# Performance work log

Measured on AMD Instinct MI355X. Metric: run time of the kernel, lower is better.

## Reference

```python
import jax, jax.numpy as jnp
import numpy as np

N, B, H, C, NF = 200000, 100, 128, 3, 128


def setup_inputs() -> dict:
    key = jax.random.key(0)
    ks = jax.random.split(key, 12)
    def w(k, shape, s=0.05):
        return jax.random.normal(k, shape, jnp.float32) * s
    return dict(
        node_feat=w(ks[0], (N, NF), 1.0),
        coord=w(ks[1], (N, 3), 1.0),
        virtual_node_feat=w(ks[2], (B, NF, C), 1.0),
        virtual_coord=w(ks[3], (B, 3, C), 1.0),
        data_batch=jnp.sort(jax.random.randint(ks[4], (N,), 0, B)),
        We1=w(ks[5], (2 * NF + 1, H)), be1=jnp.zeros((H,), jnp.float32),
        We2=w(ks[6], (H, H)), be2=jnp.zeros((H,), jnp.float32),
        Wc1=w(ks[7], (H, H)), bc1=jnp.zeros((H,), jnp.float32),
        Wc2=w(ks[8], (H, 1), 0.001),  # xavier gain=0.001 layer, no bias
        Wn1=w(ks[9], (2 * H, H)), bn1=jnp.zeros((H,), jnp.float32),
        Wn2=w(ks[10], (H, H)), bn2=jnp.zeros((H,), jnp.float32),
    )


def _segment_mean(x, idx, num_segments):
    # x: [N, d1, d2] -> [num_segments, d1, d2]; mean over nodes of each graph
    sums = jax.ops.segment_sum(x, idx, num_segments=num_segments)
    counts = jax.ops.segment_sum(jnp.ones((x.shape[0],), x.dtype), idx,
                                 num_segments=num_segments)
    return sums / jnp.maximum(counts, 1.0)[:, None, None]


def reference(node_feat, coord, virtual_node_feat, virtual_coord, data_batch,
              We1, be1, We2, be2, Wc1, bc1, Wc2, Wn1, bn1, Wn2, bn2):
    silu = jax.nn.silu
    n, nf = node_feat.shape
    nb, _, c = virtual_coord.shape

    # gather: real node -> its graph's virtual nodes
    diff = virtual_coord[data_batch] - coord[:, :, None]            # [N,3,C]
    radial = jnp.linalg.norm(diff, axis=1)                          # [N,C]

    # edge model (work in [N,C,feat] layout to avoid permutes)
    feat_R = jnp.broadcast_to(node_feat[:, None, :], (n, c, nf))    # [N,C,NF]
    feat_V = virtual_node_feat[data_batch].transpose(0, 2, 1)       # [N,C,NF]
    e_in = jnp.concatenate([feat_R, feat_V, radial[:, :, None]], axis=-1)
    m = silu(e_in @ We1 + be1)
    m = silu(m @ We2 + be2)                                         # [N,C,H]

    # coord model: per (node, virtual-channel) scalar weight
    s = silu(m @ Wc1 + bc1) @ Wc2                                   # [N,C,1]
    trans = diff * s[:, :, 0][:, None, :]                           # [N,3,C]
    virtual_coord = virtual_coord + _segment_mean(trans, data_batch, nb)

    # node model on virtual nodes
    agg = _segment_mean(m, data_batch, nb)                          # [B,C,H]
    n_in = jnp.concatenate([virtual_node_feat.transpose(0, 2, 1), agg], axis=-1)
    h = silu(n_in @ Wn1 + bn1) @ Wn2 + bn2                          # [B,C,H]
    virtual_node_feat = virtual_node_feat + h.transpose(0, 2, 1)    # residual

    return virtual_node_feat, virtual_coord
```

## Files before the change

kernel.cpp:

```cpp
#include <hip/hip_runtime.h>
#include <hip/hip_bf16.h>
#include <math.h>

#define NNODES 200000
#define NGRAPH 100
#define HD     128
#define NCH    3
#define BN     64
#define EROWS  (BN*NCH)
#define ESTR   136

typedef short short8 __attribute__((ext_vector_type(8)));
typedef float f32x4  __attribute__((ext_vector_type(4)));
typedef unsigned int u32x2 __attribute__((ext_vector_type(2)));
typedef unsigned int u32x4 __attribute__((ext_vector_type(4)));

#define MFMA_16x16x32(a,b,c) __builtin_amdgcn_mfma_f32_16x16x32_bf16((a),(b),(c),0,0,0)

__device__ __forceinline__ float bf2f(unsigned short u) {
    return __uint_as_float(((unsigned int)u) << 16);
}
__device__ __forceinline__ unsigned short f2bf(float f) {
    return (unsigned short)((__float_as_uint(f) + 0x8000u) >> 16);
}
__device__ __forceinline__ unsigned int pack2bf(float lo, float hi) {
    unsigned int a = __float_as_uint(lo) + 0x8000u;
    unsigned int b = __float_as_uint(hi) + 0x8000u;
    return __builtin_amdgcn_perm(b, a, 0x07060302u);
}
__device__ __forceinline__ short8 as_short8(u32x4 v) {
    union { u32x4 u; short8 s; } x; x.u = v; return x.s;
}
__device__ __forceinline__ float silu_f(float x) {
    return x * __builtin_amdgcn_rcpf(1.0f + __expf(-x));
}

__global__ void prep_kernel(const float* __restrict__ We1,
                            const float* __restrict__ We2,
                            const float* __restrict__ Wc1,
                            const float* __restrict__ be1,
                            const float* __restrict__ be2,
                            const float* __restrict__ bc1,
                            const float* __restrict__ Wc2,
                            const float* __restrict__ vnf,
                            unsigned short* __restrict__ w1r,
                            unsigned short* __restrict__ w2r,
                            unsigned short* __restrict__ wc1r,
                            float* __restrict__ Q,
                            float* __restrict__ wlast,
                            float* __restrict__ be1f,
                            float* __restrict__ be2f,
                            float* __restrict__ bc1f,
                            float* __restrict__ wc2f,
                            float* __restrict__ zacc) {
    int bid = blockIdx.x;
    if (bid < 192) {
        int t = bid * 256 + threadIdx.x;
        int m  = t / 16384;
        int e  = t % 16384;
        int j  = e & 7;
        int l  = (e >> 3) & 63;
        int ks = (e >> 9) & 3;
        int ct = e >> 11;
        int kf  = ks * 32 + (l >> 4) * 8 + j;
        int col = ct * 16 + (l & 15);
        int srck = (m == 0) ? kf : (((kf & 7) << 4) | (kf >> 3));
        const float*    src = (m == 0) ? We1 : ((m == 1) ? We2 : Wc1);
        unsigned short* dst = (m == 0) ? w1r : ((m == 1) ? w2r : wc1r);
        dst[e] = f2bf(src[srck * 128 + col]);
        if (t < 128) {
            wlast[t] = We1[256 * 128 + t];
            be1f[t]  = be1[t];
            be2f[t]  = be2[t];
            bc1f[t]  = bc1[t];
            wc2f[t]  = Wc2[t];
        }
    } else if (bid < 492) {
        int bc = bid - 192;
        int b = bc / NCH, c = bc % NCH;
        int t = threadIdx.x;
        __shared__ float v[128];
        if (t < 128) v[t] = vnf[(b * 128 + t) * 3 + c];
        __syncthreads();
        if (t < 128) {
            float s0 = 0.f, s1 = 0.f, s2 = 0.f, s3 = 0.f;
            for (int k = 0; k < 128; k += 4) {
                s0 += v[k + 0] * We1[(128 + k + 0) * 128 + t];
                s1 += v[k + 1] * We1[(128 + k + 1) * 128 + t];
                s2 += v[k + 2] * We1[(128 + k + 2) * 128 + t];
                s3 += v[k + 3] * We1[(128 + k + 3) * 128 + t];
            }
            Q[(b * 3 + c) * 128 + t] = (s0 + s1) + (s2 + s3);
        }
    } else {
        int idx = (bid - 492) * 256 + threadIdx.x;
        if (idx < 39400) zacc[idx] = 0.0f;
    }
}

__global__ __launch_bounds__(256, 2) void egcl_main(
    const float* __restrict__ node_feat,
    const float* __restrict__ coord,
    const float* __restrict__ vcoord,
    const int*   __restrict__ batch,
    const unsigned short* __restrict__ w1r,
    const unsigned short* __restrict__ w2r,
    const unsigned short* __restrict__ wc1r,
    const float* __restrict__ Q,
    const float* __restrict__ wlast,
    const float* __restrict__ be1f,
    const float* __restrict__ be2f,
    const float* __restrict__ bc1f,
    const float* __restrict__ wc2f,
    float* __restrict__ aggsum,
    float* __restrict__ transsum,
    float* __restrict__ cnt)
{
    __shared__ __align__(16) unsigned short e_buf[EROWS * ESTR];
    __shared__ unsigned short sbatch[BN];
    __shared__ unsigned short sseg_start[BN + 1];
    __shared__ unsigned short sseg_b[BN];
    __shared__ int snseg;

    const int tid   = threadIdx.x;
    const int wave  = tid >> 6;
    const int lane  = tid & 63;
    const int lrow  = lane & 15;
    const int lkb   = (lane >> 4) * 8;
    const int rq    = (lane >> 4) * 4;
    const int node0 = blockIdx.x * BN;

    if (tid < BN) {
        int n = node0 + tid;
        int b = batch[n];
        sbatch[tid] = (unsigned short)b;
        int prev = (tid > 0) ? batch[n - 1] : -1;
        unsigned long long mask = __ballot(b != prev);
        int ns = __popcll(mask);
        if (b != prev) {
            int idx = __popcll(mask & ((1ull << tid) - 1ull));
            sseg_start[idx] = (unsigned short)tid;
            sseg_b[idx]     = (unsigned short)b;
        }
        if (tid == 0) { sseg_start[ns] = BN; snseg = ns; }
        float cx = coord[n * 3 + 0];
        float cy = coord[n * 3 + 1];
        float cz = coord[n * 3 + 2];
        for (int c = 0; c < 3; ++c) {
            float dx = vcoord[b * 9 + 0 * 3 + c] - cx;
            float dy = vcoord[b * 9 + 1 * 3 + c] - cy;
            float dz = vcoord[b * 9 + 2 * 3 + c] - cz;
            f32x4 pad;
            pad[0] = dx; pad[1] = dy; pad[2] = dz;
            pad[3] = sqrtf(dx * dx + dy * dy + dz * dz);
            *(f32x4*)&e_buf[(c * 64 + tid) * ESTR + 128] = pad;
        }
    }
    __syncthreads();
    const int nseg = snseg;

    f32x4 acc1[8] = {};
    {
        const float* arow = node_feat + (size_t)(node0 + wave * 16 + lrow) * 128;
        for (int ks = 0; ks < 4; ++ks) {
            f32x4 x0 = *(const f32x4*)(arow + ks * 32 + lkb);
            f32x4 x1 = *(const f32x4*)(arow + ks * 32 + lkb + 4);
            u32x4 av;
            av[0] = pack2bf(x0[0], x0[1]);
            av[1] = pack2bf(x0[2], x0[3]);
            av[2] = pack2bf(x1[0], x1[1]);
            av[3] = pack2bf(x1[2], x1[3]);
            short8 af = as_short8(av);
            for (int ct = 0; ct < 8; ++ct) {
                short8 bfg = *(const short8*)(w1r + ((ct * 4 + ks) * 64 + lane) * 8);
                acc1[ct] = MFMA_16x16x32(af, bfg, acc1[ct]);
            }
        }
    }
    {
        float wl[8];
        #pragma unroll
        for (int ct = 0; ct < 8; ++ct)
            wl[ct] = wlast[ct * 16 + lrow];
        if (nseg == 1) {
            const float* qb = Q + (int)sseg_b[0] * (NCH * HD);
            float qv[3][8];
            #pragma unroll
            for (int c = 0; c < 3; ++c)
                #pragma unroll
                for (int ct = 0; ct < 8; ++ct)
                    qv[c][ct] = qb[c * 128 + ct * 16 + lrow] + be1f[ct * 16 + lrow];
            #pragma unroll
            for (int r = 0; r < 4; ++r) {
                int nl = wave * 16 + rq + r;
                #pragma unroll
                for (int c = 0; c < 3; ++c) {
                    int row = c * 64 + nl;
                    float rad = *(const float*)&e_buf[row * ESTR + 134];
                    float v[8];
                    #pragma unroll
                    for (int ct = 0; ct < 8; ++ct)
                        v[ct] = silu_f(acc1[ct][r] + qv[c][ct] + rad * wl[ct]);
                    u32x4 av;
                    av[0] = pack2bf(v[0], v[1]);
                    av[1] = pack2bf(v[2], v[3]);
                    av[2] = pack2bf(v[4], v[5]);
                    av[3] = pack2bf(v[6], v[7]);
                    *(u32x4*)&e_buf[row * ESTR + lrow * 8] = av;
                }
            }
        } else {
            float bb[8];
            #pragma unroll
            for (int ct = 0; ct < 8; ++ct)
                bb[ct] = be1f[ct * 16 + lrow];
            #pragma unroll
            for (int r = 0; r < 4; ++r) {
                int nl = wave * 16 + rq + r;
                int b  = sbatch[nl];
                #pragma unroll
                for (int c = 0; c < 3; ++c) {
                    int row = c * 64 + nl;
                    float rad = *(const float*)&e_buf[row * ESTR + 134];
                    const float* qb = Q + (b * 3 + c) * 128;
                    float v[8];
                    #pragma unroll
                    for (int ct = 0; ct < 8; ++ct)
                        v[ct] = silu_f(acc1[ct][r] + bb[ct] + qb[ct * 16 + lrow]
                                       + rad * wl[ct]);
                    u32x4 av;
                    av[0] = pack2bf(v[0], v[1]);
                    av[1] = pack2bf(v[2], v[3]);
                    av[2] = pack2bf(v[4], v[5]);
                    av[3] = pack2bf(v[6], v[7]);
                    *(u32x4*)&e_buf[row * ESTR + lrow * 8] = av;
                }
            }
        }
    }

    const int bagg = (nseg == 1) ? (int)sseg_b[0] * (NCH * HD) : 0;

    for (int half = 0; half < 2; ++half) {
        f32x4 acc[3][4] = {};
        for (int ks = 0; ks < 4; ++ks) {
            short8 af[3];
            #pragma unroll
            for (int j = 0; j < 3; ++j)
                af[j] = *(const short8*)(&e_buf[(j * 64 + wave * 16 + lrow) * ESTR +
                                                ks * 32 + lkb]);
            #pragma unroll
            for (int c4 = 0; c4 < 4; ++c4) {
                int ct = half * 4 + c4;
                short8 bfg = *(const short8*)(w2r + ((ct * 4 + ks) * 64 + lane) * 8);
                #pragma unroll
                for (int j = 0; j < 3; ++j)
                    acc[j][c4] = MFMA_16x16x32(af[j], bfg, acc[j][c4]);
            }
        }
        float b0 = be2f[(half * 4 + 0) * 16 + lrow];
        float b1 = be2f[(half * 4 + 1) * 16 + lrow];
        float b2 = be2f[(half * 4 + 2) * 16 + lrow];
        float b3 = be2f[(half * 4 + 3) * 16 + lrow];
        #pragma unroll
        for (int j = 0; j < 3; ++j) {
            float ps0 = 0.f, ps1 = 0.f, ps2 = 0.f, ps3 = 0.f;
            #pragma unroll
            for (int r = 0; r < 4; ++r) {
                int row = j * 64 + wave * 16 + rq + r;
                float v0 = silu_f(acc[j][0][r] + b0);
                float v1 = silu_f(acc[j][1][r] + b1);
                float v2 = silu_f(acc[j][2][r] + b2);
                float v3 = silu_f(acc[j][3][r] + b3);
                ps0 += v0; ps1 += v1; ps2 += v2; ps3 += v3;
                u32x2 dv;
                dv[0] = pack2bf(v0, v1);
                dv[1] = pack2bf(v2, v3);
                *(u32x2*)&e_buf[row * ESTR + lrow * 8 + half * 4] = dv;
            }
            if (nseg == 1) {
                ps0 += __shfl_xor(ps0, 16, 64); ps0 += __shfl_xor(ps0, 32, 64);
                ps1 += __shfl_xor(ps1, 16, 64); ps1 += __shfl_xor(ps1, 32, 64);
                ps2 += __shfl_xor(ps2, 16, 64); ps2 += __shfl_xor(ps2, 32, 64);
                ps3 += __shfl_xor(ps3, 16, 64); ps3 += __shfl_xor(ps3, 32, 64);
                if (lane < 16) {
                    atomicAdd(&aggsum[bagg + j * 128 + (half * 4 + 0) * 16 + lane], ps0);
                    atomicAdd(&aggsum[bagg + j * 128 + (half * 4 + 1) * 16 + lane], ps1);
                    atomicAdd(&aggsum[bagg + j * 128 + (half * 4 + 2) * 16 + lane], ps2);
                    atomicAdd(&aggsum[bagg + j * 128 + (half * 4 + 3) * 16 + lane], ps3);
                }
            }
        }
    }

    float p[3][4] = {};
    for (int half = 0; half < 2; ++half) {
        f32x4 acc[3][4] = {};
        for (int ks = 0; ks < 4; ++ks) {
            short8 af[3];
            #pragma unroll
            for (int j = 0; j < 3; ++j)
                af[j] = *(const short8*)(&e_buf[(j * 64 + wave * 16 + lrow) * ESTR +
                                                ks * 32 + lkb]);
            #pragma unroll
            for (int c4 = 0; c4 < 4; ++c4) {
                int ct = half * 4 + c4;
                short8 bfg = *(const short8*)(wc1r + ((ct * 4 + ks) * 64 + lane) * 8);
                #pragma unroll
                for (int j = 0; j < 3; ++j)
                    acc[j][c4] = MFMA_16x16x32(af[j], bfg, acc[j][c4]);
            }
        }
        float b0 = bc1f[(half * 4 + 0) * 16 + lrow];
        float b1 = bc1f[(half * 4 + 1) * 16 + lrow];
        float b2 = bc1f[(half * 4 + 2) * 16 + lrow];
        float b3 = bc1f[(half * 4 + 3) * 16 + lrow];
        float w0 = wc2f[(half * 4 + 0) * 16 + lrow];
        float w1 = wc2f[(half * 4 + 1) * 16 + lrow];
        float w2 = wc2f[(half * 4 + 2) * 16 + lrow];
        float w3 = wc2f[(half * 4 + 3) * 16 + lrow];
        #pragma unroll
        for (int j = 0; j < 3; ++j) {
            #pragma unroll
            for (int r = 0; r < 4; ++r) {
                float s = p[j][r];
                s += silu_f(acc[j][0][r] + b0) * w0;
                s += silu_f(acc[j][1][r] + b1) * w1;
                s += silu_f(acc[j][2][r] + b2) * w2;
                s += silu_f(acc[j][3][r] + b3) * w3;
                p[j][r] = s;
            }
        }
    }
    for (int j = 0; j < 3; ++j) {
        float p0 = p[j][0], p1 = p[j][1], p2 = p[j][2], p3 = p[j][3];
        #pragma unroll
        for (int off = 1; off < 16; off <<= 1) {
            p0 += __shfl_xor(p0, off, 64);
            p1 += __shfl_xor(p1, off, 64);
            p2 += __shfl_xor(p2, off, 64);
            p3 += __shfl_xor(p3, off, 64);
        }
        if (lrow == 0) {
            int rbase = j * 64 + wave * 16 + rq;
            *(float*)&e_buf[(rbase + 0) * ESTR + 134] = p0;
            *(float*)&e_buf[(rbase + 1) * ESTR + 134] = p1;
            *(float*)&e_buf[(rbase + 2) * ESTR + 134] = p2;
            *(float*)&e_buf[(rbase + 3) * ESTR + 134] = p3;
        }
    }
    __syncthreads();

    if (nseg == 1) {
        int b = sseg_b[0];
        if (wave == 0) {
            float t[9];
            #pragma unroll
            for (int c = 0; c < 3; ++c) {
                int row = c * 64 + lane;
                float sv = *(const float*)&e_buf[row * ESTR + 134];
                float dx = *(const float*)&e_buf[row * ESTR + 128];
                float dy = *(const float*)&e_buf[row * ESTR + 130];
                float dz = *(const float*)&e_buf[row * ESTR + 132];
                t[0 * 3 + c] = dx * sv;
                t[1 * 3 + c] = dy * sv;
                t[2 * 3 + c] = dz * sv;
            }
            #pragma unroll
            for (int off = 1; off < 64; off <<= 1)
                #pragma unroll
                for (int k = 0; k < 9; ++k)
                    t[k] += __shfl_xor(t[k], off, 64);
            if (lane < 9)
                atomicAdd(&transsum[b * 9 + lane],
                          __shfl(t[lane], 0, 64));
            if (lane == 0) atomicAdd(&cnt[b], 64.0f);
        }
    } else {
        for (int sg = 0; sg < nseg; ++sg) {
            int s0 = sseg_start[sg], s1 = sseg_start[sg + 1], b = sseg_b[sg];
            for (int idx = tid; idx < NCH * HD; idx += 256) {
                int c = idx >> 7, pcol = idx & 127;
                float sum = 0.f;
                for (int ii = s0; ii < s1; ++ii)
                    sum += bf2f(e_buf[(c * 64 + ii) * ESTR + pcol]);
                int h = ((pcol & 7) << 4) | (pcol >> 3);
                atomicAdd(&aggsum[(b * 3 + c) * 128 + h], sum);
            }
            if (tid < 9) {
                int d = tid / 3, c = tid % 3;
                float sum = 0.f;
                for (int ii = s0; ii < s1; ++ii)
                    sum += (*(const float*)&e_buf[(c * 64 + ii) * ESTR + 128 + 2 * d])
                           * (*(const float*)&e_buf[(c * 64 + ii) * ESTR + 134]);
                atomicAdd(&transsum[b * 9 + d * 3 + c], sum);
            }
            if (tid == 0) atomicAdd(&cnt[b], (float)(s1 - s0));
        }
    }
}

__global__ void finalize_kernel(const float* __restrict__ vnf,
                                const float* __restrict__ vcoord,
                                const float* __restrict__ Wn1,
                                const float* __restrict__ bn1,
                                const float* __restrict__ Wn2,
                                const float* __restrict__ bn2,
                                const float* __restrict__ aggsum,
                                const float* __restrict__ transsum,
                                const float* __restrict__ cnt,
                                float* __restrict__ out) {
    int b = blockIdx.x / NCH;
    int c = blockIdx.x % NCH;
    int j = threadIdx.x;
    __shared__ float nin[256];
    __shared__ float h1[128];
    float count = fmaxf(cnt[b], 1.0f);
    nin[j]       = vnf[(b * 128 + j) * 3 + c];
    nin[128 + j] = aggsum[(b * 3 + c) * 128 + j] / count;
    __syncthreads();
    float x0 = bn1[j], x1 = 0.f, x2 = 0.f, x3 = 0.f;
    for (int k = 0; k < 256; k += 4) {
        x0 += nin[k + 0] * Wn1[(k + 0) * 128 + j];
        x1 += nin[k + 1] * Wn1[(k + 1) * 128 + j];
        x2 += nin[k + 2] * Wn1[(k + 2) * 128 + j];
        x3 += nin[k + 3] * Wn1[(k + 3) * 128 + j];
    }
    h1[j] = silu_f((x0 + x1) + (x2 + x3));
    __syncthreads();
    float y0 = bn2[j], y1 = 0.f, y2 = 0.f, y3 = 0.f;
    for (int k = 0; k < 128; k += 4) {
        y0 += h1[k + 0] * Wn2[(k + 0) * 128 + j];
        y1 += h1[k + 1] * Wn2[(k + 1) * 128 + j];
        y2 += h1[k + 2] * Wn2[(k + 2) * 128 + j];
        y3 += h1[k + 3] * Wn2[(k + 3) * 128 + j];
    }
    float y = (y0 + y1) + (y2 + y3);
    out[(b * 128 + j) * 3 + c] = vnf[(b * 128 + j) * 3 + c] + y;
    if (c == 0 && j < 9) {
        out[NGRAPH * 128 * 3 + b * 9 + j] =
            vcoord[b * 9 + j] + transsum[b * 9 + j] / count;
    }
}

extern "C" void kernel_launch(void* const* d_in, const int* in_sizes, int n_in,
                              void* d_out, int out_size, void* d_ws, size_t ws_size,
                              hipStream_t stream) {
    const float* node_feat = (const float*)d_in[0];
    const float* coord     = (const float*)d_in[1];
    const float* vnf       = (const float*)d_in[2];
    const float* vcoord    = (const float*)d_in[3];
    const int*   batch     = (const int*)d_in[4];
    const float* We1 = (const float*)d_in[5];
    const float* be1 = (const float*)d_in[6];
    const float* We2 = (const float*)d_in[7];
    const float* be2 = (const float*)d_in[8];
    const float* Wc1 = (const float*)d_in[9];
    const float* bc1 = (const float*)d_in[10];
    const float* Wc2 = (const float*)d_in[11];
    const float* Wn1 = (const float*)d_in[12];
    const float* bn1 = (const float*)d_in[13];
    const float* Wn2 = (const float*)d_in[14];
    const float* bn2 = (const float*)d_in[15];

    char* ws = (char*)d_ws;
    float*          aggsum   = (float*)(ws + 0);
    float*          transsum = (float*)(ws + 153600);
    float*          cntp     = (float*)(ws + 157200);
    float*          Q        = (float*)(ws + 157600);
    unsigned short* w1r      = (unsigned short*)(ws + 311200);
    unsigned short* w2r      = (unsigned short*)(ws + 343968);
    unsigned short* wc1r     = (unsigned short*)(ws + 376736);
    float*          wlast    = (float*)(ws + 409504);
    float*          be1f     = (float*)(ws + 410016);
    float*          be2f     = (float*)(ws + 410528);
    float*          bc1f     = (float*)(ws + 411040);
    float*          wc2f     = (float*)(ws + 411552);

    prep_kernel<<<192 + NGRAPH * NCH + 154, 256, 0, stream>>>(
        We1, We2, Wc1, be1, be2, bc1, Wc2, vnf,
        w1r, w2r, wc1r, Q, wlast, be1f, be2f, bc1f, wc2f,
        (float*)ws);

    egcl_main<<<NNODES / BN, 256, 0, stream>>>(
        node_feat, coord, vcoord, batch, w1r, w2r, wc1r, Q,
        wlast, be1f, be2f, bc1f, wc2f, aggsum, transsum, cntp);

    finalize_kernel<<<NGRAPH * NCH, 128, 0, stream>>>(
        vnf, vcoord, Wn1, bn1, Wn2, bn2, aggsum, transsum, cntp,
        (float*)d_out);
}
```

Before: 299.4 us.

## Shrink LDS footprint by processing channel 2 in a second pass

The edge staging buffer drops from three channel planes to two. The third channel's layer-1 output is held in registers and processed after channels 0 and 1 finish layer 2 and the coord MLP. Radial and diff values and the per-row scalars move into small separate float buffers. The aim is to cut shared memory per block so more blocks fit per CU and register pressure in the MFMA loops falls, at the cost of redoing the weight loads for a third pass and adding extra barriers when a tile holds several segments.

```diff
diff --git a/kernel.cpp b/kernel.cpp
--- a/kernel.cpp
+++ b/kernel.cpp
@@ -9,6 +9,7 @@
 #define BN     64
 #define EROWS  (BN*NCH)
 #define ESTR   136
+#define PL     (BN*ESTR)
 
 typedef short short8 __attribute__((ext_vector_type(8)));
 typedef float f32x4  __attribute__((ext_vector_type(4)));
@@ -116,7 +117,9 @@
     float* __restrict__ transsum,
     float* __restrict__ cnt)
 {
-    __shared__ __align__(16) unsigned short e_buf[EROWS * ESTR];
+    __shared__ __align__(16) unsigned short planes[2][PL];
+    __shared__ __align__(16) float pad_buf[EROWS * 4];
+    __shared__ float s_vals[EROWS];
     __shared__ unsigned short sbatch[BN];
     __shared__ unsigned short sseg_start[BN + 1];
     __shared__ unsigned short sseg_b[BN];
@@ -129,6 +132,7 @@
     const int lkb   = (lane >> 4) * 8;
     const int rq    = (lane >> 4) * 4;
     const int node0 = blockIdx.x * BN;
+    const int myrow = wave * 16 + lrow;
 
     if (tid < BN) {
         int n = node0 + tid;
@@ -153,7 +157,7 @@
             f32x4 pad;
             pad[0] = dx; pad[1] = dy; pad[2] = dz;
             pad[3] = sqrtf(dx * dx + dy * dy + dz * dz);
-            *(f32x4*)&e_buf[(c * 64 + tid) * ESTR + 128] = pad;
+            *(f32x4*)&pad_buf[(c * 64 + tid) * 4] = pad;
         }
     }
     __syncthreads();
@@ -161,7 +165,7 @@
 
     f32x4 acc1[8] = {};
     {
-        const float* arow = node_feat + (size_t)(node0 + wave * 16 + lrow) * 128;
+        const float* arow = node_feat + (size_t)(node0 + myrow) * 128;
         for (int ks = 0; ks < 4; ++ks) {
             f32x4 x0 = *(const f32x4*)(arow + ks * 32 + lkb);
             f32x4 x1 = *(const f32x4*)(arow + ks * 32 + lkb + 4);
@@ -177,13 +181,17 @@
             }
         }
     }
+
+    const int bagg = (nseg == 1) ? (int)sseg_b[0] * (NCH * HD) : 0;
+
+    u32x4 e2r[4];
     {
         float wl[8];
         #pragma unroll
         for (int ct = 0; ct < 8; ++ct)
             wl[ct] = wlast[ct * 16 + lrow];
         if (nseg == 1) {
-            const float* qb = Q + (int)sseg_b[0] * (NCH * HD);
+            const float* qb = Q + bagg;
             float qv[3][8];
             #pragma unroll
             for (int c = 0; c < 3; ++c)
@@ -195,8 +203,7 @@
                 int nl = wave * 16 + rq + r;
                 #pragma unroll
                 for (int c = 0; c < 3; ++c) {
-                    int row = c * 64 + nl;
-                    float rad = *(const float*)&e_buf[row * ESTR + 134];
+                    float rad = pad_buf[(c * 64 + nl) * 4 + 3];
                     float v[8];
                     #pragma unroll
                     for (int ct = 0; ct < 8; ++ct)
@@ -206,7 +213,8 @@
                     av[1] = pack2bf(v[2], v[3]);
                     av[2] = pack2bf(v[4], v[5]);
                     av[3] = pack2bf(v[6], v[7]);
-                    *(u32x4*)&e_buf[row * ESTR + lrow * 8] = av;
+                    if (c < 2) *(u32x4*)&planes[c][nl * ESTR + lrow * 8] = av;
+                    else       e2r[r] = av;
                 }
             }
         } else {
@@ -220,8 +228,7 @@
                 int b  = sbatch[nl];
                 #pragma unroll
                 for (int c = 0; c < 3; ++c) {
-                    int row = c * 64 + nl;
-                    float rad = *(const float*)&e_buf[row * ESTR + 134];
+                    float rad = pad_buf[(c * 64 + nl) * 4 + 3];
                     const float* qb = Q + (b * 3 + c) * 128;
                     float v[8];
                     #pragma unroll
@@ -233,29 +240,25 @@
                     av[1] = pack2bf(v[2], v[3]);
                     av[2] = pack2bf(v[4], v[5]);
                     av[3] = pack2bf(v[6], v[7]);
-                    *(u32x4*)&e_buf[row * ESTR + lrow * 8] = av;
+                    if (c < 2) *(u32x4*)&planes[c][nl * ESTR + lrow * 8] = av;
+                    else       e2r[r] = av;
                 }
             }
         }
     }
-
-    const int bagg = (nseg == 1) ? (int)sseg_b[0] * (NCH * HD) : 0;
+    asm volatile("" ::: "memory");
 
     for (int half = 0; half < 2; ++half) {
-        f32x4 acc[3][4] = {};
+        f32x4 acc[2][4] = {};
         for (int ks = 0; ks < 4; ++ks) {
-            short8 af[3];
-            #pragma unroll
-            for (int j = 0; j < 3; ++j)
-                af[j] = *(const short8*)(&e_buf[(j * 64 + wave * 16 + lrow) * ESTR +
-                                                ks * 32 + lkb]);
+            short8 af0 = *(const short8*)&planes[0][myrow * ESTR + ks * 32 + lkb];
+            short8 af1 = *(const short8*)&planes[1][myrow * ESTR + ks * 32 + lkb];
             #pragma unroll
             for (int c4 = 0; c4 < 4; ++c4) {
                 int ct = half * 4 + c4;
                 short8 bfg = *(const short8*)(w2r + ((ct * 4 + ks) * 64 + lane) * 8);
-                #pragma unroll
-                for (int j = 0; j < 3; ++j)
-                    acc[j][c4] = MFMA_16x16x32(af[j], bfg, acc[j][c4]);
+                acc[0][c4] = MFMA_16x16x32(af0, bfg, acc[0][c4]);
+                acc[1][c4] = MFMA_16x16x32(af1, bfg, acc[1][c4]);
             }
         }
         float b0 = be2f[(half * 4 + 0) * 16 + lrow];
@@ -263,11 +266,11 @@
         float b2 = be2f[(half * 4 + 2) * 16 + lrow];
         float b3 = be2f[(half * 4 + 3) * 16 + lrow];
         #pragma unroll
-        for (int j = 0; j < 3; ++j) {
+        for (int j = 0; j < 2; ++j) {
             float ps0 = 0.f, ps1 = 0.f, ps2 = 0.f, ps3 = 0.f;
             #pragma unroll
             for (int r = 0; r < 4; ++r) {
-                int row = j * 64 + wave * 16 + rq + r;
+                int nl = wave * 16 + rq + r;
                 float v0 = silu_f(acc[j][0][r] + b0);
                 float v1 = silu_f(acc[j][1][r] + b1);
                 float v2 = silu_f(acc[j][2][r] + b2);
@@ -276,7 +279,7 @@
                 u32x2 dv;
                 dv[0] = pack2bf(v0, v1);
                 dv[1] = pack2bf(v2, v3);
-                *(u32x2*)&e_buf[row * ESTR + lrow * 8 + half * 4] = dv;
+                *(u32x2*)&planes[j][nl * ESTR + lrow * 8 + half * 4] = dv;
             }
             if (nseg == 1) {
                 ps0 += __shfl_xor(ps0, 16, 64); ps0 += __shfl_xor(ps0, 32, 64);
@@ -292,48 +295,148 @@
             }
         }
     }
-
-    float p[3][4] = {};
-    for (int half = 0; half < 2; ++half) {
-        f32x4 acc[3][4] = {};
+    asm volatile("" ::: "memory");
+
+    {
+        float p[2][4] = {};
+        for (int half = 0; half < 2; ++half) {
+            f32x4 acc[2][4] = {};
+            for (int ks = 0; ks < 4; ++ks) {
+                short8 af0 = *(const short8*)&planes[0][myrow * ESTR + ks * 32 + lkb];
+                short8 af1 = *(const short8*)&planes[1][myrow * ESTR + ks * 32 + lkb];
+                #pragma unroll
+                for (int c4 = 0; c4 < 4; ++c4) {
+                    int ct = half * 4 + c4;
+                    short8 bfg = *(const short8*)(wc1r + ((ct * 4 + ks) * 64 + lane) * 8);
+                    acc[0][c4] = MFMA_16x16x32(af0, bfg, acc[0][c4]);
+                    acc[1][c4] = MFMA_16x16x32(af1, bfg, acc[1][c4]);
+                }
+            }
+            float b0 = bc1f[(half * 4 + 0) * 16 + lrow];
+            float b1 = bc1f[(half * 4 + 1) * 16 + lrow];
+            float b2 = bc1f[(half * 4 + 2) * 16 + lrow];
+            float b3 = bc1f[(half * 4 + 3) * 16 + lrow];
+            float w0 = wc2f[(half * 4 + 0) * 16 + lrow];
+            float w1 = wc2f[(half * 4 + 1) * 16 + lrow];
+            float w2 = wc2f[(half * 4 + 2) * 16 + lrow];
+            float w3 = wc2f[(half * 4 + 3) * 16 + lrow];
+            #pragma unroll
+            for (int j = 0; j < 2; ++j) {
+                #pragma unroll
+                for (int r = 0; r < 4; ++r) {
+                    float s = p[j][r];
+                    s += silu_f(acc[j][0][r] + b0) * w0;
+                    s += silu_f(acc[j][1][r] + b1) * w1;
+                    s += silu_f(acc[j][2][r] + b2) * w2;
+                    s += silu_f(acc[j][3][r] + b3) * w3;
+                    p[j][r] = s;
+                }
+            }
+        }
+        #pragma unroll
+        for (int j = 0; j < 2; ++j) {
+            float p0 = p[j][0], p1 = p[j][1], p2 = p[j][2], p3 = p[j][3];
+            #pragma unroll
+            for (int off = 1; off < 16; off <<= 1) {
+                p0 += __shfl_xor(p0, off, 64);
+                p1 += __shfl_xor(p1, off, 64);
+                p2 += __shfl_xor(p2, off, 64);
+                p3 += __shfl_xor(p3, off, 64);
+            }
+            if (lrow == 0) {
+                int rbase = j * 64 + wave * 16 + rq;
+                s_vals[rbase + 0] = p0;
+                s_vals[rbase + 1] = p1;
+                s_vals[rbase + 2] = p2;
+                s_vals[rbase + 3] = p3;
+            }
+        }
+    }
+
+    if (nseg > 1) {
+        __syncthreads();
+        for (int sg = 0; sg < nseg; ++sg) {
+            int s0 = sseg_start[sg], s1 = sseg_start[sg + 1], b = sseg_b[sg];
+            int cj = tid >> 7, pcol = tid & 127;
+            float sum = 0.f;
+            for (int ii = s0; ii < s1; ++ii)
+                sum += bf2f(planes[cj][ii * ESTR + pcol]);
+            int h = ((pcol & 7) << 4) | (pcol >> 3);
+            atomicAdd(&aggsum[(b * 3 + cj) * 128 + h], sum);
+        }
+        __syncthreads();
+    }
+    asm volatile("" ::: "memory");
+
+    #pragma unroll
+    for (int r = 0; r < 4; ++r) {
+        int nl = wave * 16 + rq + r;
+        *(u32x4*)&planes[0][nl * ESTR + lrow * 8] = e2r[r];
+    }
+    asm volatile("" ::: "memory");
+    {
+        f32x4 acc2[8] = {};
         for (int ks = 0; ks < 4; ++ks) {
-            short8 af[3];
-            #pragma unroll
-            for (int j = 0; j < 3; ++j)
-                af[j] = *(const short8*)(&e_buf[(j * 64 + wave * 16 + lrow) * ESTR +
-                                                ks * 32 + lkb]);
-            #pragma unroll
-            for (int c4 = 0; c4 < 4; ++c4) {
-                int ct = half * 4 + c4;
+            short8 af = *(const short8*)&planes[0][myrow * ESTR + ks * 32 + lkb];
+            #pragma unroll
+            for (int ct = 0; ct < 8; ++ct) {
+                short8 bfg = *(const short8*)(w2r + ((ct * 4 + ks) * 64 + lane) * 8);
+                acc2[ct] = MFMA_16x16x32(af, bfg, acc2[ct]);
+            }
+        }
+        float psum[8];
+        #pragma unroll
+        for (int ct = 0; ct < 8; ++ct) psum[ct] = 0.0f;
+        #pragma unroll
+        for (int r = 0; r < 4; ++r) {
+            int nl = wave * 16 + rq + r;
+            float v[8];
+            #pragma unroll
+            for (int ct = 0; ct < 8; ++ct) {
+                v[ct] = silu_f(acc2[ct][r] + be2f[ct * 16 + lrow]);
+                psum[ct] += v[ct];
+            }
+            u32x4 av;
+            av[0] = pack2bf(v[0], v[1]);
+            av[1] = pack2bf(v[2], v[3]);
+            av[2] = pack2bf(v[4], v[5]);
+            av[3] = pack2bf(v[6], v[7]);
+            *(u32x4*)&planes[0][nl * ESTR + lrow * 8] = av;
+        }
+        if (nseg == 1) {
+            #pragma unroll
+            for (int ct = 0; ct < 8; ++ct) {
+                psum[ct] += __shfl_xor(psum[ct], 16, 64);
+                psum[ct] += __shfl_xor(psum[ct], 32, 64);
+            }
+            if (lane < 16) {
+                #pragma unroll
+                for (int ct = 0; ct < 8; ++ct)
+                    atomicAdd(&aggsum[bagg + 2 * 128 + ct * 16 + lane], psum[ct]);
+            }
+        }
+    }
+    asm volatile("" ::: "memory");
+    {
+        f32x4 acc3[8] = {};
+        for (int ks = 0; ks < 4; ++ks) {
+            short8 af = *(const short8*)&planes[0][myrow * ESTR + ks * 32 + lkb];
+            #pragma unroll
+            for (int ct = 0; ct < 8; ++ct) {
                 short8 bfg = *(const short8*)(wc1r + ((ct * 4 + ks) * 64 + lane) * 8);
-                #pragma unroll
-                for (int j = 0; j < 3; ++j)
-                    acc[j][c4] = MFMA_16x16x32(af[j], bfg, acc[j][c4]);
-            }
-        }
-        float b0 = bc1f[(half * 4 + 0) * 16 + lrow];
-        float b1 = bc1f[(half * 4 + 1) * 16 + lrow];
-        float b2 = bc1f[(half * 4 + 2) * 16 + lrow];
-        float b3 = bc1f[(half * 4 + 3) * 16 + lrow];
-        float w0 = wc2f[(half * 4 + 0) * 16 + lrow];
-        float w1 = wc2f[(half * 4 + 1) * 16 + lrow];
-        float w2 = wc2f[(half * 4 + 2) * 16 + lrow];
-        float w3 = wc2f[(half * 4 + 3) * 16 + lrow];
+                acc3[ct] = MFMA_16x16x32(af, bfg, acc3[ct]);
+            }
+        }
+        float p0 = 0.f, p1 = 0.f, p2 = 0.f, p3 = 0.f;
         #pragma unroll
-        for (int j = 0; j < 3; ++j) {
-            #pragma unroll
-            for (int r = 0; r < 4; ++r) {
-                float s = p[j][r];
-                s += silu_f(acc[j][0][r] + b0) * w0;
-                s += silu_f(acc[j][1][r] + b1) * w1;
-                s += silu_f(acc[j][2][r] + b2) * w2;
-                s += silu_f(acc[j][3][r] + b3) * w3;
-                p[j][r] = s;
-            }
-        }
-    }
-    for (int j = 0; j < 3; ++j) {
-        float p0 = p[j][0], p1 = p[j][1], p2 = p[j][2], p3 = p[j][3];
+        for (int ct = 0; ct < 8; ++ct) {
+            float bb = bc1f[ct * 16 + lrow];
+            float w2 = wc2f[ct * 16 + lrow];
+            p0 += silu_f(acc3[ct][0] + bb) * w2;
+            p1 += silu_f(acc3[ct][1] + bb) * w2;
+            p2 += silu_f(acc3[ct][2] + bb) * w2;
+            p3 += silu_f(acc3[ct][3] + bb) * w2;
+        }
         #pragma unroll
         for (int off = 1; off < 16; off <<= 1) {
             p0 += __shfl_xor(p0, off, 64);
@@ -342,11 +445,26 @@
             p3 += __shfl_xor(p3, off, 64);
         }
         if (lrow == 0) {
-            int rbase = j * 64 + wave * 16 + rq;
-            *(float*)&e_buf[(rbase + 0) * ESTR + 134] = p0;
-            *(float*)&e_buf[(rbase + 1) * ESTR + 134] = p1;
-            *(float*)&e_buf[(rbase + 2) * ESTR + 134] = p2;
-            *(float*)&e_buf[(rbase + 3) * ESTR + 134] = p3;
+            int rbase = 2 * 64 + wave * 16 + rq;
+            s_vals[rbase + 0] = p0;
+            s_vals[rbase + 1] = p1;
+            s_vals[rbase + 2] = p2;
+            s_vals[rbase + 3] = p3;
+        }
+    }
+
+    if (nseg > 1) {
+        __syncthreads();
+        for (int sg = 0; sg < nseg; ++sg) {
+            int s0 = sseg_start[sg], s1 = sseg_start[sg + 1], b = sseg_b[sg];
+            if (tid < 128) {
+                int pcol = tid;
+                float sum = 0.f;
+                for (int ii = s0; ii < s1; ++ii)
+                    sum += bf2f(planes[0][ii * ESTR + pcol]);
+                int h = ((pcol & 7) << 4) | (pcol >> 3);
+                atomicAdd(&aggsum[(b * 3 + 2) * 128 + h], sum);
+            }
         }
     }
     __syncthreads();
@@ -357,14 +475,11 @@
             float t[9];
             #pragma unroll
             for (int c = 0; c < 3; ++c) {
-                int row = c * 64 + lane;
-                float sv = *(const float*)&e_buf[row * ESTR + 134];
-                float dx = *(const float*)&e_buf[row * ESTR + 128];
-                float dy = *(const float*)&e_buf[row * ESTR + 130];
-                float dz = *(const float*)&e_buf[row * ESTR + 132];
-                t[0 * 3 + c] = dx * sv;
-                t[1 * 3 + c] = dy * sv;
-                t[2 * 3 + c] = dz * sv;
+                f32x4 pd = *(const f32x4*)&pad_buf[(c * 64 + lane) * 4];
+                float sv = s_vals[c * 64 + lane];
+                t[0 * 3 + c] = pd[0] * sv;
+                t[1 * 3 + c] = pd[1] * sv;
+                t[2 * 3 + c] = pd[2] * sv;
             }
             #pragma unroll
             for (int off = 1; off < 64; off <<= 1)
@@ -377,25 +492,20 @@
             if (lane == 0) atomicAdd(&cnt[b], 64.0f);
         }
     } else {
-        for (int sg = 0; sg < nseg; ++sg) {
-            int s0 = sseg_start[sg], s1 = sseg_start[sg + 1], b = sseg_b[sg];
-            for (int idx = tid; idx < NCH * HD; idx += 256) {
-                int c = idx >> 7, pcol = idx & 127;
+        if (tid < 9) {
+            int d = tid / 3, c = tid % 3;
+            for (int sg = 0; sg < nseg; ++sg) {
+                int s0 = sseg_start[sg], s1 = sseg_start[sg + 1], b = sseg_b[sg];
                 float sum = 0.f;
                 for (int ii = s0; ii < s1; ++ii)
-                    sum += bf2f(e_buf[(c * 64 + ii) * ESTR + pcol]);
-                int h = ((pcol & 7) << 4) | (pcol >> 3);
-                atomicAdd(&aggsum[(b * 3 + c) * 128 + h], sum);
-            }
-            if (tid < 9) {
-                int d = tid / 3, c = tid % 3;
-                float sum = 0.f;
-                for (int ii = s0; ii < s1; ++ii)
-                    sum += (*(const float*)&e_buf[(c * 64 + ii) * ESTR + 128 + 2 * d])
-                           * (*(const float*)&e_buf[(c * 64 + ii) * ESTR + 134]);
+                    sum += pad_buf[(c * 64 + ii) * 4 + d] * s_vals[c * 64 + ii];
                 atomicAdd(&transsum[b * 9 + d * 3 + c], sum);
             }
-            if (tid == 0) atomicAdd(&cnt[b], (float)(s1 - s0));
+        }
+        if (tid == 0) {
+            for (int sg = 0; sg < nseg; ++sg)
+                atomicAdd(&cnt[sseg_b[sg]],
+                          (float)(sseg_start[sg + 1] - sseg_start[sg]));
         }
     }
 }
```

Result: slower. 340.0 us (+13.6%).
